# Kernel optimization log

Measured on AMD Instinct MI355X. Metric: run time of the kernel, lower is better.

## Reference

```python
import jax, jax.numpy as jnp
import numpy as np

N, S, D, DOUT, ATTEN, NUM_ATTR = 10000, 20, 512, 512, 64, 9

def setup_inputs() -> dict:
    key = jax.random.key(0)
    ks = jax.random.split(key, 9)
    return {
        "self_vecs": jax.random.normal(ks[0], (N, D), dtype=jnp.float32),
        "neigh_vecs": jax.random.normal(ks[1], (N, S, D), dtype=jnp.float32),
        "neigh_weight": jax.random.uniform(ks[2], (N, S, 1), dtype=jnp.float32),
        "neigh_column": jax.random.randint(ks[3], (N, S, 1), 0, NUM_ATTR, dtype=jnp.int32),
        "neigh_weights": jax.random.normal(ks[4], (D, DOUT), dtype=jnp.float32) * (1.0 / np.sqrt(D)),
        "self_weights": jax.random.normal(ks[5], (D, DOUT), dtype=jnp.float32) * (1.0 / np.sqrt(D)),
        "alpha": jax.random.normal(ks[6], (NUM_ATTR,), dtype=jnp.float32),
        "self_atten": jax.random.normal(ks[7], (D, ATTEN), dtype=jnp.float32) * (1.0 / np.sqrt(D)),
        "neigh_atten": jax.random.normal(ks[8], (D, ATTEN), dtype=jnp.float32) * (1.0 / np.sqrt(D)),
        "v": jax.random.normal(jax.random.fold_in(key, 99), (ATTEN, 1), dtype=jnp.float32) * (1.0 / np.sqrt(ATTEN)),
    }

def reference(self_vecs, neigh_vecs, neigh_weight, neigh_column,
              neigh_weights, self_weights, alpha, self_atten, neigh_atten, v):
    # per-neighbor edge weighting
    nv = neigh_vecs * neigh_weight                      # [N,S,D]
    # gather alpha by attribute column, softmax over neighbors (axis=1)
    a = alpha[neigh_column[..., 0]][..., None]          # [N,S,1]
    a_exp = jnp.exp(a)
    atten = a_exp / jnp.sum(a_exp, axis=1, keepdims=True)
    nv = nv * atten
    # dropout = 0.0 -> identity
    neigh_sum = jnp.sum(nv, axis=1)                     # [N,D]
    from_neighs = neigh_sum @ neigh_weights             # [N,DOUT]
    from_self = self_vecs @ self_weights                # [N,DOUT]
    self_ai = self_vecs @ self_atten                    # [N,ATTEN]
    neigh_ai = neigh_sum @ neigh_atten                  # [N,ATTEN]
    imp_self = self_ai + self_ai
    imp_neigh = neigh_ai + self_ai
    a_self = jnp.exp(jnp.tanh(imp_self @ v))            # [N,1]
    a_neigh = jnp.exp(jnp.tanh(imp_neigh @ v))          # [N,1]
    denom = a_self + a_neigh
    out = (a_self / denom) * from_self + (a_neigh / denom) * from_neighs
    return jax.nn.relu(out)
```

## Files before the change

### kernel.cpp

```cpp
#include <hip/hip_runtime.h>
#include <hip/hip_bf16.h>

#define N_NODES 10000
#define S_NB 20
#define D_IN 512
#define D_OUT 512
#define ATTEN_D 64
#define KTOT 1024
#define M_PAD 10048

typedef __bf16 bf16_t;
typedef bf16_t bf16x8 __attribute__((ext_vector_type(8)));
typedef float f32x4 __attribute__((ext_vector_type(4)));

__device__ __forceinline__ unsigned short f2bf(float f) {
    unsigned int u = __float_as_uint(f);
    unsigned int r = u + 0x7FFFu + ((u >> 16) & 1u);
    return (unsigned short)(r >> 16);
}

__device__ __forceinline__ void gl_lds16(const unsigned short* g, unsigned short* l) {
    __builtin_amdgcn_global_load_lds(
        (const __attribute__((address_space(1))) void*)g,
        (__attribute__((address_space(3))) void*)l,
        16, 0, 0);
}

__global__ void prep_kernel(const float* __restrict__ neigh_w,
                            const float* __restrict__ self_w,
                            const float* __restrict__ self_atten,
                            const float* __restrict__ neigh_atten,
                            const float* __restrict__ v,
                            float* __restrict__ u_self, float* __restrict__ u_neigh,
                            unsigned short* __restrict__ Wt,
                            unsigned short* __restrict__ X) {
    int idx = blockIdx.x * blockDim.x + threadIdx.x;
    int stride = gridDim.x * blockDim.x;

    for (int i = idx; i < D_OUT * KTOT; i += stride) {
        int n = i >> 10;
        int k = i & (KTOT - 1);
        float w = (k < D_IN) ? self_w[k * D_OUT + n] : neigh_w[(k - D_IN) * D_OUT + n];
        Wt[i] = f2bf(w);
    }
    for (int i = idx; i < 2 * D_IN; i += stride) {
        const float* row = (i < D_IN) ? (self_atten + (size_t)i * ATTEN_D)
                                      : (neigh_atten + (size_t)(i - D_IN) * ATTEN_D);
        float s = 0.f;
        #pragma unroll
        for (int j = 0; j < ATTEN_D; ++j) s = fmaf(row[j], v[j], s);
        if (i < D_IN) u_self[i] = s; else u_neigh[i - D_IN] = s;
    }
    for (int i = idx; i < (M_PAD - N_NODES) * KTOT; i += stride) {
        X[(size_t)N_NODES * KTOT + i] = 0;
    }
}

__global__ __launch_bounds__(128) void aggregate_kernel(
        const float* __restrict__ self_vecs, const float* __restrict__ neigh_vecs,
        const float* __restrict__ neigh_weight, const int* __restrict__ neigh_column,
        const float* __restrict__ alpha,
        const float* __restrict__ u_self, const float* __restrict__ u_neigh,
        unsigned short* __restrict__ X) {
    const int n = blockIdx.x;
    const int tid = threadIdx.x;

    __shared__ float coef[S_NB];
    __shared__ float ew[2 * S_NB];
    __shared__ float red[4];
    __shared__ float gates[2];

    if (tid < S_NB) {
        int col = neigh_column[n * S_NB + tid];
        ew[tid] = expf(alpha[col]);
        ew[S_NB + tid] = neigh_weight[n * S_NB + tid];
    }
    __syncthreads();
    if (tid == 0) {
        float s = 0.f;
        for (int i = 0; i < S_NB; ++i) s += ew[i];
        float inv = 1.0f / s;
        for (int i = 0; i < S_NB; ++i) coef[i] = ew[S_NB + i] * ew[i] * inv;
    }
    __syncthreads();

    const float4* nb = (const float4*)(neigh_vecs + (size_t)n * S_NB * D_IN);
    float4 acc = make_float4(0.f, 0.f, 0.f, 0.f);
    #pragma unroll
    for (int s = 0; s < S_NB; ++s) {
        float4 t = nb[s * 128 + tid];
        float c = coef[s];
        acc.x = fmaf(c, t.x, acc.x);
        acc.y = fmaf(c, t.y, acc.y);
        acc.z = fmaf(c, t.z, acc.z);
        acc.w = fmaf(c, t.w, acc.w);
    }
    float4 sv = ((const float4*)(self_vecs + (size_t)n * D_IN))[tid];
    float4 us = ((const float4*)u_self)[tid];
    float4 un = ((const float4*)u_neigh)[tid];
    float p1 = sv.x * us.x + sv.y * us.y + sv.z * us.z + sv.w * us.w;
    float p2 = acc.x * un.x + acc.y * un.y + acc.z * un.z + acc.w * un.w;

    #pragma unroll
    for (int off = 32; off > 0; off >>= 1) {
        p1 += __shfl_down(p1, off, 64);
        p2 += __shfl_down(p2, off, 64);
    }
    int lane = tid & 63, wid = tid >> 6;
    if (lane == 0) { red[wid * 2] = p1; red[wid * 2 + 1] = p2; }
    __syncthreads();
    if (tid == 0) {
        float s1 = red[0] + red[2];
        float s2 = red[1] + red[3];
        float a_s = expf(tanhf(2.0f * s1));
        float a_n = expf(tanhf(s2 + s1));
        float inv = 1.0f / (a_s + a_n);
        gates[0] = a_s * inv;
        gates[1] = a_n * inv;
    }
    __syncthreads();
    float gs = gates[0], gn = gates[1];

    unsigned short* xrow = X + (size_t)n * KTOT;
    ushort4 o;
    o.x = f2bf(gs * sv.x); o.y = f2bf(gs * sv.y);
    o.z = f2bf(gs * sv.z); o.w = f2bf(gs * sv.w);
    *(ushort4*)(xrow + tid * 4) = o;
    o.x = f2bf(gn * acc.x); o.y = f2bf(gn * acc.y);
    o.z = f2bf(gn * acc.z); o.w = f2bf(gn * acc.w);
    *(ushort4*)(xrow + D_IN + tid * 4) = o;
}

#define BM 64
#define BN 128
#define BK 32

__global__ __launch_bounds__(256) void gemm_kernel(
        const unsigned short* __restrict__ X, const unsigned short* __restrict__ Wt,
        float* __restrict__ out) {
    __shared__ __align__(16) unsigned short As[BM * BK];
    __shared__ __align__(16) unsigned short Bs[BN * BK];
    const int tid = threadIdx.x;
    const int lane = tid & 63;
    const int wid = tid >> 6;
    const int m0 = blockIdx.y * BM;
    const int n0 = blockIdx.x * BN;
    const int wm = (wid >> 1) * 32;
    const int wn = (wid & 1) * 64;
    const int quad = lane >> 4;
    const int mrow = lane & 15;

    f32x4 acc[2][4];
    f32x4 zero = {0.f, 0.f, 0.f, 0.f};
    #pragma unroll
    for (int i = 0; i < 2; ++i)
        #pragma unroll
        for (int j = 0; j < 4; ++j) acc[i][j] = zero;

    const int lr = lane >> 2;
    const int lk = (lane & 3) * 8;
    const unsigned short* gA  = X  + (size_t)(m0 + wid * 16 + lr) * KTOT + lk;
    const unsigned short* gB0 = Wt + (size_t)(n0 + wid * 32 + lr) * KTOT + lk;
    const unsigned short* gB1 = Wt + (size_t)(n0 + wid * 32 + 16 + lr) * KTOT + lk;
    unsigned short* lA  = As + wid * 512 + lane * 8;
    unsigned short* lB0 = Bs + wid * 1024 + lane * 8;
    unsigned short* lB1 = Bs + wid * 1024 + 512 + lane * 8;

    for (int k0 = 0; k0 < KTOT; k0 += BK) {
        __syncthreads();
        gl_lds16(gA + k0, lA);
        gl_lds16(gB0 + k0, lB0);
        gl_lds16(gB1 + k0, lB1);
        __syncthreads();

        bf16x8 a[2], b[4];
        #pragma unroll
        for (int i = 0; i < 2; ++i)
            a[i] = *(const bf16x8*)(As + (wm + i * 16 + mrow) * BK + quad * 8);
        #pragma unroll
        for (int j = 0; j < 4; ++j)
            b[j] = *(const bf16x8*)(Bs + (wn + j * 16 + mrow) * BK + quad * 8);
        #pragma unroll
        for (int i = 0; i < 2; ++i)
            #pragma unroll
            for (int j = 0; j < 4; ++j)
                acc[i][j] = __builtin_amdgcn_mfma_f32_16x16x32_bf16(a[i], b[j], acc[i][j], 0, 0, 0);
    }

    #pragma unroll
    for (int i = 0; i < 2; ++i) {
        int rbase = m0 + wm + i * 16 + quad * 4;
        #pragma unroll
        for (int j = 0; j < 4; ++j) {
            int c = n0 + wn + j * 16 + mrow;
            #pragma unroll
            for (int r = 0; r < 4; ++r) {
                int R = rbase + r;
                if (R < N_NODES)
                    out[(size_t)R * D_OUT + c] = fmaxf(acc[i][j][r], 0.f);
            }
        }
    }
}

extern "C" void kernel_launch(void* const* d_in, const int* in_sizes, int n_in,
                              void* d_out, int out_size, void* d_ws, size_t ws_size,
                              hipStream_t stream) {
    const float* self_vecs     = (const float*)d_in[0];
    const float* neigh_vecs    = (const float*)d_in[1];
    const float* neigh_weight  = (const float*)d_in[2];
    const int*   neigh_column  = (const int*)d_in[3];
    const float* neigh_weights = (const float*)d_in[4];
    const float* self_weights  = (const float*)d_in[5];
    const float* alpha         = (const float*)d_in[6];
    const float* self_atten    = (const float*)d_in[7];
    const float* neigh_atten   = (const float*)d_in[8];
    const float* v             = (const float*)d_in[9];
    float* out = (float*)d_out;

    char* ws = (char*)d_ws;
    float* u_self  = (float*)ws;
    float* u_neigh = u_self + D_IN;
    unsigned short* Wt = (unsigned short*)(ws + 4096);
    unsigned short* X  = (unsigned short*)(ws + 4096 + (size_t)D_OUT * KTOT * 2);

    hipLaunchKernelGGL(prep_kernel, dim3(256), dim3(256), 0, stream,
                       neigh_weights, self_weights, self_atten, neigh_atten, v,
                       u_self, u_neigh, Wt, X);
    hipLaunchKernelGGL(aggregate_kernel, dim3(N_NODES), dim3(128), 0, stream,
                       self_vecs, neigh_vecs, neigh_weight, neigh_column, alpha,
                       u_self, u_neigh, X);
    hipLaunchKernelGGL(gemm_kernel, dim3(D_OUT / BN, M_PAD / BM), dim3(256), 0, stream,
                       X, Wt, out);
}
```

Baseline: 596.2 us.

## Double GEMM K-tile, use warp-shuffle softmax in aggregate, widen prep grid

The GEMM K tile grows from 32 to 64. All 256 threads now cooperatively stage A and B rows into LDS, and each barrier pair is followed by two MFMA sub-steps, which halves the number of barrier-bound iterations. The aggregate kernel replaces the serial single-thread softmax with a wavefront shuffle reduction, removing one barrier. The prep kernel launches four times as many blocks. Larger LDS tiles may introduce bank conflicts because rows now use a stride of 64 bf16 elements with no padding.

```diff
diff --git a/kernel.cpp b/kernel.cpp
--- a/kernel.cpp
+++ b/kernel.cpp
@@ -66,21 +66,20 @@
     const int tid = threadIdx.x;
 
     __shared__ float coef[S_NB];
-    __shared__ float ew[2 * S_NB];
     __shared__ float red[4];
     __shared__ float gates[2];
 
-    if (tid < S_NB) {
-        int col = neigh_column[n * S_NB + tid];
-        ew[tid] = expf(alpha[col]);
-        ew[S_NB + tid] = neigh_weight[n * S_NB + tid];
-    }
-    __syncthreads();
-    if (tid == 0) {
-        float s = 0.f;
-        for (int i = 0; i < S_NB; ++i) s += ew[i];
-        float inv = 1.0f / s;
-        for (int i = 0; i < S_NB; ++i) coef[i] = ew[S_NB + i] * ew[i] * inv;
+    if (tid < 64) {
+        float e = 0.f, wgt = 0.f;
+        if (tid < S_NB) {
+            e = expf(alpha[neigh_column[n * S_NB + tid]]);
+            wgt = neigh_weight[n * S_NB + tid];
+        }
+        float s = e;
+        #pragma unroll
+        for (int off = 32; off > 0; off >>= 1) s += __shfl_down(s, off, 64);
+        s = __shfl(s, 0, 64);
+        if (tid < S_NB) coef[tid] = wgt * e / s;
     }
     __syncthreads();
 
@@ -133,7 +132,7 @@
 
 #define BM 64
 #define BN 128
-#define BK 32
+#define BK 64
 
 __global__ __launch_bounds__(256) void gemm_kernel(
         const unsigned short* __restrict__ X, const unsigned short* __restrict__ Wt,
@@ -157,34 +156,46 @@
         #pragma unroll
         for (int j = 0; j < 4; ++j) acc[i][j] = zero;
 
-    const int lr = lane >> 2;
-    const int lk = (lane & 3) * 8;
-    const unsigned short* gA  = X  + (size_t)(m0 + wid * 16 + lr) * KTOT + lk;
-    const unsigned short* gB0 = Wt + (size_t)(n0 + wid * 32 + lr) * KTOT + lk;
-    const unsigned short* gB1 = Wt + (size_t)(n0 + wid * 32 + 16 + lr) * KTOT + lk;
-    unsigned short* lA  = As + wid * 512 + lane * 8;
-    unsigned short* lB0 = Bs + wid * 1024 + lane * 8;
-    unsigned short* lB1 = Bs + wid * 1024 + 512 + lane * 8;
+    const int srow = tid >> 3;
+    const int skp  = (tid & 7) * 8;
+    const unsigned short* gA0 = X  + (size_t)(m0 + srow) * KTOT + skp;
+    const unsigned short* gA1 = X  + (size_t)(m0 + 32 + srow) * KTOT + skp;
+    const unsigned short* gB0 = Wt + (size_t)(n0 + srow) * KTOT + skp;
+    const unsigned short* gB1 = Wt + (size_t)(n0 + 32 + srow) * KTOT + skp;
+    const unsigned short* gB2 = Wt + (size_t)(n0 + 64 + srow) * KTOT + skp;
+    const unsigned short* gB3 = Wt + (size_t)(n0 + 96 + srow) * KTOT + skp;
+    unsigned short* lA0 = As + tid * 8;
+    unsigned short* lA1 = As + 2048 + tid * 8;
+    unsigned short* lB0 = Bs + tid * 8;
+    unsigned short* lB1 = Bs + 2048 + tid * 8;
+    unsigned short* lB2 = Bs + 4096 + tid * 8;
+    unsigned short* lB3 = Bs + 6144 + tid * 8;
 
     for (int k0 = 0; k0 < KTOT; k0 += BK) {
         __syncthreads();
-        gl_lds16(gA + k0, lA);
+        gl_lds16(gA0 + k0, lA0);
+        gl_lds16(gA1 + k0, lA1);
         gl_lds16(gB0 + k0, lB0);
         gl_lds16(gB1 + k0, lB1);
+        gl_lds16(gB2 + k0, lB2);
+        gl_lds16(gB3 + k0, lB3);
         __syncthreads();
 
-        bf16x8 a[2], b[4];
-        #pragma unroll
-        for (int i = 0; i < 2; ++i)
-            a[i] = *(const bf16x8*)(As + (wm + i * 16 + mrow) * BK + quad * 8);
-        #pragma unroll
-        for (int j = 0; j < 4; ++j)
-            b[j] = *(const bf16x8*)(Bs + (wn + j * 16 + mrow) * BK + quad * 8);
-        #pragma unroll
-        for (int i = 0; i < 2; ++i)
+        #pragma unroll
+        for (int s = 0; s < 2; ++s) {
+            bf16x8 a[2], b[4];
+            #pragma unroll
+            for (int i = 0; i < 2; ++i)
+                a[i] = *(const bf16x8*)(As + (wm + i * 16 + mrow) * BK + s * 32 + quad * 8);
             #pragma unroll
             for (int j = 0; j < 4; ++j)
-                acc[i][j] = __builtin_amdgcn_mfma_f32_16x16x32_bf16(a[i], b[j], acc[i][j], 0, 0, 0);
+                b[j] = *(const bf16x8*)(Bs + (wn + j * 16 + mrow) * BK + s * 32 + quad * 8);
+            #pragma unroll
+            for (int i = 0; i < 2; ++i)
+                #pragma unroll
+                for (int j = 0; j < 4; ++j)
+                    acc[i][j] = __builtin_amdgcn_mfma_f32_16x16x32_bf16(a[i], b[j], acc[i][j], 0, 0, 0);
+        }
     }
 
     #pragma unroll
@@ -224,7 +235,7 @@
     unsigned short* Wt = (unsigned short*)(ws + 4096);
     unsigned short* X  = (unsigned short*)(ws + 4096 + (size_t)D_OUT * KTOT * 2);
 
-    hipLaunchKernelGGL(prep_kernel, dim3(256), dim3(256), 0, stream,
+    hipLaunchKernelGGL(prep_kernel, dim3(1024), dim3(256), 0, stream,
                        neigh_weights, self_weights, self_atten, neigh_atten, v,
                        u_self, u_neigh, Wt, X);
     hipLaunchKernelGGL(aggregate_kernel, dim3(N_NODES), dim3(128), 0, stream,
```

After: 595.5 us. Within noise of the previous version (-0.1%).
